# Kernel optimization log

Measured on AMD Instinct MI355X. Metric: run time of the kernel, lower is better.

The kernel has to match this reference:

```python
import jax, jax.numpy as jnp
import numpy as np
import math

B, S, D, H = 2, 2048, 1024, 16
DK = D // H

def setup_inputs() -> dict:
    key = jax.random.key(0)
    ks = jax.random.split(key, 12)
    std = 1.0 / math.sqrt(D)
    inp = {
        'query': jax.random.normal(ks[0], (B, S, D), jnp.float32),
        'key':   jax.random.normal(ks[1], (B, S, D), jnp.float32),
        'value': jax.random.normal(ks[2], (B, S, D), jnp.float32),
        'mask':  jnp.ones((B, 1, 1, S), dtype=bool),
        'wq': jax.random.normal(ks[3], (D, D), jnp.float32) * std,
        'bq': jnp.zeros((D,), jnp.float32),
        'wk': jax.random.normal(ks[4], (D, D), jnp.float32) * std,
        'bk': jnp.zeros((D,), jnp.float32),
        'wv': jax.random.normal(ks[5], (D, D), jnp.float32) * std,
        'bv': jnp.zeros((D,), jnp.float32),
        'wo': jax.random.normal(ks[6], (D, D), jnp.float32) * std,
        'bo': jnp.zeros((D,), jnp.float32),
    }
    return inp

def reference(query, key, value, mask, wq, bq, wk, bk, wv, bv, wo, bo):
    # torch.nn.Linear: y = x @ W^T + b
    def split_heads(x):  # [B,S,D] -> [B,H,S,DK]
        return x.reshape(B, -1, H, DK).transpose(0, 2, 1, 3)
    Q = split_heads(query @ wq.T + bq)
    K = split_heads(key @ wk.T + bk)
    V = split_heads(value @ wv.T + bv)
    scale = 1.0 / math.sqrt(DK)
    scores = jnp.einsum('bhtd,bhsd->bhts', Q, K * scale)  # [B,H,S,S]
    scores = jnp.where(mask, scores, -jnp.inf)
    attn = jax.nn.softmax(scores, axis=-1)
    # dropout p=0.0 (eval) -> identity
    context = jnp.einsum('bhts,bhsd->bhtd', attn, V)
    context = context.transpose(0, 2, 1, 3).reshape(B, -1, D)
    return context @ wo.T + bo
```

## Files before the change

kernel.cpp:

```cpp
#include <hip/hip_runtime.h>
#include <stdint.h>

#define SEQ 2048
#define NH  16

typedef __bf16 bf16x8 __attribute__((ext_vector_type(8)));
typedef float  f32x4  __attribute__((ext_vector_type(4)));
typedef float  f32x16 __attribute__((ext_vector_type(16)));
typedef unsigned uint2v __attribute__((ext_vector_type(2)));

#if __has_builtin(__builtin_amdgcn_exp2f)
#define EXP2(x) __builtin_amdgcn_exp2f(x)
#else
#define EXP2(x) exp2f(x)
#endif

#define WAITV0 asm volatile("s_waitcnt vmcnt(0)" ::: "memory")
#define WAITV4 asm volatile("s_waitcnt vmcnt(4)" ::: "memory")
#define SBAR() do { __builtin_amdgcn_sched_barrier(0); __builtin_amdgcn_s_barrier(); __builtin_amdgcn_sched_barrier(0); } while (0)

__device__ __forceinline__ unsigned short f2bf(float f) {
  union { float f; uint32_t u; } v; v.f = f;
  uint32_t r = v.u + 0x7fffu + ((v.u >> 16) & 1u);
  return (unsigned short)(r >> 16);
}

__device__ __forceinline__ void gll16(const void* g, void* l) {
  __builtin_amdgcn_global_load_lds((const __attribute__((address_space(1))) void*)g,
                                   (__attribute__((address_space(3))) void*)l, 16, 0, 0);
}

__device__ __forceinline__ f32x4 mfma16(bf16x8 a, bf16x8 b, f32x4 c) {
  return __builtin_amdgcn_mfma_f32_16x16x32_bf16(a, b, c, 0, 0, 0);
}
__device__ __forceinline__ f32x16 mfma32(bf16x8 a, bf16x8 b, f32x16 c) {
  return __builtin_amdgcn_mfma_f32_32x32x16_bf16(a, b, c, 0, 0, 0);
}

struct CvtJobs {
  const float* s[7];
  unsigned short* d[7];
  int n4[7];
};

__global__ void cvt_all(CvtJobs J) {
  int j = blockIdx.y;
  const float* __restrict__ s = J.s[j];
  unsigned short* __restrict__ d = J.d[j];
  int n4 = J.n4[j];
  int st = gridDim.x * blockDim.x;
  for (int i = blockIdx.x * blockDim.x + threadIdx.x; i < n4; i += st) {
    float4 v = ((const float4*)s)[i];
    union { unsigned short u[4]; uint2 q; } o;
    o.u[0] = f2bf(v.x); o.u[1] = f2bf(v.y); o.u[2] = f2bf(v.z); o.u[3] = f2bf(v.w);
    ((uint2*)d)[i] = o.q;
  }
}

struct GemmJobs {
  const unsigned short* A[3];
  const unsigned short* W[3];
  const float* bias[3];
  void* out[3];
  float scale[3];
  int mode[3];
};

template<int BM, int NB>
__global__ __launch_bounds__(256, (BM == 128 ? 3 : 2)) void gemm_t(GemmJobs J) {
  __shared__ alignas(16) unsigned short Asm[BM * 64];
  __shared__ alignas(16) unsigned short Bsm[128 * 64];
  constexpr int MFR = BM / 32;
  constexpr int MB = 4096 / BM;
  const int tid = threadIdx.x;
  const int l = tid & 63, w = tid >> 6;
  const int wr = w >> 1, wc = w & 1;
  const int lg = l >> 4, lo = l & 15;

  const int nwg = gridDim.x;
  const int id = blockIdx.x;
  const int swz = (id & 7) * (nwg >> 3) + (id >> 3);
  const int g = swz / NB;
  const int rem = swz % NB;
  const int m0 = (rem % MB) * BM;
  const int n0 = (rem / MB) * 128;

  const unsigned short* __restrict__ A = J.A[g];
  const unsigned short* __restrict__ W = J.W[g];
  const float* __restrict__ bias = J.bias[g];
  const int mode = J.mode[g];
  const float scale = J.scale[g];

  f32x4 acc[MFR][4] = {};

  for (int kt = 0; kt < 16; ++kt) {
#pragma unroll
    for (int it = 0; it < BM / 32; ++it) {
      int chunk = it * 256 + tid;
      int row = chunk >> 3, c = chunk & 7;
      const char* src = (const char*)A + (((size_t)(m0 + row) << 10) + (kt << 6)) * 2 + ((c ^ (row & 7)) << 4);
      gll16(src, (char*)Asm + ((it * 256 + (tid & ~63)) << 4));
    }
#pragma unroll
    for (int it = 0; it < 4; ++it) {
      int chunk = it * 256 + tid;
      int row = chunk >> 3, c = chunk & 7;
      const char* src = (const char*)W + (((size_t)(n0 + row) << 10) + (kt << 6)) * 2 + ((c ^ (row & 7)) << 4);
      gll16(src, (char*)Bsm + ((it * 256 + (tid & ~63)) << 4));
    }
    WAITV0;
    SBAR();
#pragma unroll
    for (int kf = 0; kf < 2; ++kf) {
      bf16x8 af[MFR], bfr[4];
#pragma unroll
      for (int mf = 0; mf < MFR; ++mf) {
        int row = wr * (BM / 2) + mf * 16 + lo;
        int pos = (kf * 4 + lg) ^ (row & 7);
        af[mf] = *(const bf16x8*)((const char*)Asm + row * 128 + pos * 16);
      }
#pragma unroll
      for (int nf = 0; nf < 4; ++nf) {
        int row = wc * 64 + nf * 16 + lo;
        int pos = (kf * 4 + lg) ^ (row & 7);
        bfr[nf] = *(const bf16x8*)((const char*)Bsm + row * 128 + pos * 16);
      }
#pragma unroll
      for (int mf = 0; mf < MFR; ++mf)
#pragma unroll
        for (int nf = 0; nf < 4; ++nf)
          acc[mf][nf] = mfma16(af[mf], bfr[nf], acc[mf][nf]);
    }
    SBAR();
  }

#pragma unroll
  for (int mf = 0; mf < MFR; ++mf)
#pragma unroll
    for (int nf = 0; nf < 4; ++nf) {
      int gcol = n0 + wc * 64 + nf * 16 + lo;
      float bv = bias[gcol];
#pragma unroll
      for (int r = 0; r < 4; ++r) {
        int grow = m0 + wr * (BM / 2) + mf * 16 + lg * 4 + r;
        float v = (acc[mf][nf][r] + bv) * scale;
        if (mode == 2) {
          ((float*)J.out[g])[((size_t)grow << 10) + gcol] = v;
        } else {
          int b = grow >> 11, s = grow & 2047, h = gcol >> 6, dk = gcol & 63;
          size_t idx;
          if (mode == 0) idx = ((((size_t)((b << 4) + h) << 11) + s) << 6) + dk;
          else           idx = ((((size_t)((b << 4) + h) << 6) + dk) << 11) + s;
          ((__bf16*)J.out[g])[idx] = (__bf16)v;
        }
      }
    }
}

__global__ __launch_bounds__(256, 2) void attn_kernel(const unsigned short* __restrict__ Qb,
                                                      const unsigned short* __restrict__ Kb,
                                                      const unsigned short* __restrict__ Vt,
                                                      unsigned short* __restrict__ ctx) {
  __shared__ alignas(16) unsigned short Ksm[2][64 * 64];
  __shared__ alignas(16) unsigned short Vsm[2][64 * 64];
  const int tid = threadIdx.x;
  const int l = tid & 63, w = tid >> 6;
  const int ql = l & 31, hi = l >> 5;

  const int id = blockIdx.x;
  const int swz = (id & 7) * 64 + (id >> 3);
  const int bh = swz >> 4;
  const int qt = swz & 15;

  const unsigned short* Qp = Qb + (size_t)bh * SEQ * 64;
  const unsigned short* Kp = Kb + (size_t)bh * SEQ * 64;
  const unsigned short* Vp = Vt + (size_t)bh * 64 * SEQ;
  const int q0 = qt * 128 + w * 32;

  bf16x8 qb[4];
#pragma unroll
  for (int c = 0; c < 4; ++c)
    qb[c] = *(const bf16x8*)((const char*)Qp + (((size_t)(q0 + ql)) << 7) + c * 32 + hi * 16);
  WAITV0;

  f32x16 o0 = {}, o1 = {};
  float m_ = -1e30f, l_ = 0.f;

#define ASTAGE(b, t)                                                                      \
  do {                                                                                    \
    const int kv0s = (t) << 6;                                                            \
    _Pragma("unroll")                                                                     \
    for (int it = 0; it < 2; ++it) {                                                      \
      int chunk = it * 256 + tid;                                                         \
      int row = chunk >> 3, c = chunk & 7;                                                \
      const char* ksrc = (const char*)Kp + ((size_t)(kv0s + row) << 7) + ((c ^ (row & 7)) << 4); \
      gll16(ksrc, (char*)Ksm[b] + ((it * 256 + (tid & ~63)) << 4));                       \
      const char* vsrc = (const char*)Vp + ((size_t)row << 12) + (kv0s << 1) + ((c ^ (row & 7)) << 4); \
      gll16(vsrc, (char*)Vsm[b] + ((it * 256 + (tid & ~63)) << 4));                       \
    }                                                                                     \
  } while (0)

  ASTAGE(0, 0);

  for (int t = 0; t < SEQ / 64; ++t) {
    const int cur = t & 1;
    if (t < SEQ / 64 - 1) {
      ASTAGE(cur ^ 1, t + 1);
      WAITV4;
    } else {
      WAITV0;
    }
    SBAR();

    f32x16 s0 = {}, s1 = {};
    __builtin_amdgcn_s_setprio(1);
#pragma unroll
    for (int c = 0; c < 4; ++c) {
      int pr = c * 2 + hi;
      bf16x8 k0 = *(const bf16x8*)((const char*)Ksm[cur] + ql * 128 + ((pr ^ (ql & 7)) << 4));
      bf16x8 k1 = *(const bf16x8*)((const char*)Ksm[cur] + (32 + ql) * 128 + ((pr ^ ((32 + ql) & 7)) << 4));
      s0 = mfma32(k0, qb[c], s0);
      s1 = mfma32(k1, qb[c], s1);
    }
    __builtin_amdgcn_s_setprio(0);

#define MAX4(v, i) fmaxf(fmaxf(v[i], v[i+1]), fmaxf(v[i+2], v[i+3]))
    float mA = fmaxf(fmaxf(MAX4(s0, 0), MAX4(s0, 4)), fmaxf(MAX4(s0, 8), MAX4(s0, 12)));
    float mB = fmaxf(fmaxf(MAX4(s1, 0), MAX4(s1, 4)), fmaxf(MAX4(s1, 8), MAX4(s1, 12)));
    float mx = fmaxf(mA, mB);
    mx = fmaxf(mx, __shfl_xor(mx, 32));
#undef MAX4

    if (__any((int)(mx > m_))) {
      float mnew = fmaxf(m_, mx);
      float fac = EXP2(m_ - mnew);
      m_ = mnew;
#pragma unroll
      for (int r = 0; r < 16; ++r) { s0[r] = EXP2(s0[r] - mnew); s1[r] = EXP2(s1[r] - mnew); }
#define SUM4(v, i) ((v[i] + v[i+1]) + (v[i+2] + v[i+3]))
      float ps = ((SUM4(s0, 0) + SUM4(s0, 4)) + (SUM4(s0, 8) + SUM4(s0, 12)))
               + ((SUM4(s1, 0) + SUM4(s1, 4)) + (SUM4(s1, 8) + SUM4(s1, 12)));
      ps += __shfl_xor(ps, 32);
      l_ = l_ * fac + ps;
#pragma unroll
      for (int reg = 0; reg < 16; ++reg) {
        int qrow = (reg & 3) + 8 * (reg >> 2) + 4 * hi;
        float fb = __shfl(fac, qrow);
        o0[reg] *= fb; o1[reg] *= fb;
      }
    } else {
#pragma unroll
      for (int r = 0; r < 16; ++r) { s0[r] = EXP2(s0[r] - m_); s1[r] = EXP2(s1[r] - m_); }
      float ps = ((SUM4(s0, 0) + SUM4(s0, 4)) + (SUM4(s0, 8) + SUM4(s0, 12)))
               + ((SUM4(s1, 0) + SUM4(s1, 4)) + (SUM4(s1, 8) + SUM4(s1, 12)));
      ps += __shfl_xor(ps, 32);
      l_ += ps;
#undef SUM4
    }

    bf16x8 pa[4];
#pragma unroll
    for (int c = 0; c < 4; ++c) {
      const int rb = (c & 1) * 8;
      float e0, e1, e2, e3, e4, e5, e6, e7;
      if ((c >> 1) == 0) { e0=s0[rb]; e1=s0[rb+1]; e2=s0[rb+2]; e3=s0[rb+3]; e4=s0[rb+4]; e5=s0[rb+5]; e6=s0[rb+6]; e7=s0[rb+7]; }
      else               { e0=s1[rb]; e1=s1[rb+1]; e2=s1[rb+2]; e3=s1[rb+3]; e4=s1[rb+4]; e5=s1[rb+5]; e6=s1[rb+6]; e7=s1[rb+7]; }
      unsigned X0, X1, Z0, Z1;
      asm("v_cvt_pk_bf16_f32 %0, %1, %2" : "=v"(X0) : "v"(e0), "v"(e1));
      asm("v_cvt_pk_bf16_f32 %0, %1, %2" : "=v"(X1) : "v"(e2), "v"(e3));
      asm("v_cvt_pk_bf16_f32 %0, %1, %2" : "=v"(Z0) : "v"(e4), "v"(e5));
      asm("v_cvt_pk_bf16_f32 %0, %1, %2" : "=v"(Z1) : "v"(e6), "v"(e7));
      uint2v rA = __builtin_amdgcn_permlane32_swap(X0, Z0, false, false);
      uint2v rB = __builtin_amdgcn_permlane32_swap(X1, Z1, false, false);
      union { unsigned u[4]; bf16x8 v; } pk_;
      pk_.u[0] = rA[0]; pk_.u[1] = rB[0]; pk_.u[2] = rA[1]; pk_.u[3] = rB[1];
      pa[c] = pk_.v;
    }

    __builtin_amdgcn_s_setprio(1);
#pragma unroll
    for (int c = 0; c < 4; ++c) {
      int pr = c * 2 + hi;
      bf16x8 v0 = *(const bf16x8*)((const char*)Vsm[cur] + ql * 128 + ((pr ^ (ql & 7)) << 4));
      bf16x8 v1 = *(const bf16x8*)((const char*)Vsm[cur] + (32 + ql) * 128 + ((pr ^ ((32 + ql) & 7)) << 4));
      o0 = mfma32(pa[c], v0, o0);
      o1 = mfma32(pa[c], v1, o1);
    }
    __builtin_amdgcn_s_setprio(0);
    SBAR();
  }
#undef ASTAGE

  const int b = bh >> 4, h = bh & 15;
#pragma unroll
  for (int reg = 0; reg < 16; ++reg) {
    int qrow = (reg & 3) + 8 * (reg >> 2) + 4 * hi;
    float lr = __shfl(l_, qrow);
    float inv = 1.f / lr;
    int srow = q0 + qrow;
    size_t off = (((size_t)(b * SEQ + srow)) << 10) + h * 64 + ql;
    ((__bf16*)ctx)[off]      = (__bf16)(o0[reg] * inv);
    ((__bf16*)ctx)[off + 32] = (__bf16)(o1[reg] * inv);
  }
}

extern "C" void kernel_launch(void* const* d_in, const int* in_sizes, int n_in,
                              void* d_out, int out_size, void* d_ws, size_t ws_size,
                              hipStream_t stream) {
  const float* query = (const float*)d_in[0];
  const float* key_  = (const float*)d_in[1];
  const float* value = (const float*)d_in[2];
  const float* wq = (const float*)d_in[4];
  const float* bq = (const float*)d_in[5];
  const float* wk = (const float*)d_in[6];
  const float* bk = (const float*)d_in[7];
  const float* wv = (const float*)d_in[8];
  const float* bv = (const float*)d_in[9];
  const float* wo = (const float*)d_in[10];
  const float* bo = (const float*)d_in[11];

  char* ws = (char*)d_ws;
  unsigned short* xq  = (unsigned short*)(ws + 0);
  unsigned short* xk  = (unsigned short*)(ws + 8388608);
  unsigned short* xv  = (unsigned short*)(ws + 16777216);
  unsigned short* wqb = (unsigned short*)(ws + 25165824);
  unsigned short* wkb = (unsigned short*)(ws + 27262976);
  unsigned short* wvb = (unsigned short*)(ws + 29360128);
  unsigned short* wob = (unsigned short*)(ws + 31457280);
  unsigned short* Qb  = (unsigned short*)(ws + 33554432);
  unsigned short* Kb  = (unsigned short*)(ws + 41943040);
  unsigned short* Vb  = (unsigned short*)(ws + 50331648);
  unsigned short* ctx = (unsigned short*)(ws + 58720256);

  CvtJobs cj;
  cj.s[0] = query; cj.d[0] = xq;  cj.n4[0] = 1048576;
  cj.s[1] = key_;  cj.d[1] = xk;  cj.n4[1] = 1048576;
  cj.s[2] = value; cj.d[2] = xv;  cj.n4[2] = 1048576;
  cj.s[3] = wq;    cj.d[3] = wqb; cj.n4[3] = 262144;
  cj.s[4] = wk;    cj.d[4] = wkb; cj.n4[4] = 262144;
  cj.s[5] = wv;    cj.d[5] = wvb; cj.n4[5] = 262144;
  cj.s[6] = wo;    cj.d[6] = wob; cj.n4[6] = 262144;
  cvt_all<<<dim3(256, 7), 256, 0, stream>>>(cj);

  const float kscale = 0.125f * 1.44269504088896340736f;
  GemmJobs gj;
  gj.A[0] = xq; gj.W[0] = wqb; gj.bias[0] = bq; gj.out[0] = (void*)Qb; gj.scale[0] = 1.0f;   gj.mode[0] = 0;
  gj.A[1] = xk; gj.W[1] = wkb; gj.bias[1] = bk; gj.out[1] = (void*)Kb; gj.scale[1] = kscale; gj.mode[1] = 0;
  gj.A[2] = xv; gj.W[2] = wvb; gj.bias[2] = bv; gj.out[2] = (void*)Vb; gj.scale[2] = 1.0f;   gj.mode[2] = 1;
  gemm_t<128, 256><<<768, 256, 0, stream>>>(gj);

  attn_kernel<<<512, 256, 0, stream>>>(Qb, Kb, Vb, ctx);

  GemmJobs oj;
  oj.A[0] = ctx; oj.W[0] = wob; oj.bias[0] = bo; oj.out[0] = d_out; oj.scale[0] = 1.0f; oj.mode[0] = 2;
  oj.A[1] = oj.A[0]; oj.W[1] = oj.W[0]; oj.bias[1] = oj.bias[0]; oj.out[1] = oj.out[0]; oj.scale[1] = 1.0f; oj.mode[1] = 2;
  oj.A[2] = oj.A[0]; oj.W[2] = oj.W[0]; oj.bias[2] = oj.bias[0]; oj.out[2] = oj.out[0]; oj.scale[2] = 1.0f; oj.mode[2] = 2;
  gemm_t<64, 512><<<512, 256, 0, stream>>>(oj);
}
```

Baseline: 150.4 us.

## Software-pipeline QK^T one tile ahead of softmax and PV in attention loop

Restructures the flash-attention main loop so the QK^T MFMAs for the next KV tile are issued before the softmax and PV of the current tile, with the loop unrolled by two over the double buffers. The aim is to overlap MFMA work with the exp/max/convert VALU work. It also adds a lazy rescale threshold (the max is updated only when it grows by more than 8 in log2 units) and fmax3-based reductions. The costs are higher register pressure from holding two score tiles, and a stricter wait (vmcnt(0)) placed right before each barrier, which may expose load latency.

```diff
diff --git a/kernel.cpp b/kernel.cpp
--- a/kernel.cpp
+++ b/kernel.cpp
@@ -16,13 +16,16 @@
 #endif
 
 #define WAITV0 asm volatile("s_waitcnt vmcnt(0)" ::: "memory")
-#define WAITV4 asm volatile("s_waitcnt vmcnt(4)" ::: "memory")
 #define SBAR() do { __builtin_amdgcn_sched_barrier(0); __builtin_amdgcn_s_barrier(); __builtin_amdgcn_sched_barrier(0); } while (0)
 
 __device__ __forceinline__ unsigned short f2bf(float f) {
   union { float f; uint32_t u; } v; v.f = f;
   uint32_t r = v.u + 0x7fffu + ((v.u >> 16) & 1u);
   return (unsigned short)(r >> 16);
+}
+
+__device__ __forceinline__ float fmax3(float a, float b, float c) {
+  return fmaxf(fmaxf(a, b), c);
 }
 
 __device__ __forceinline__ void gll16(const void* g, void* l) {
@@ -200,48 +203,32 @@
     }                                                                                     \
   } while (0)
 
-  ASTAGE(0, 0);
-
-  for (int t = 0; t < SEQ / 64; ++t) {
-    const int cur = t & 1;
-    if (t < SEQ / 64 - 1) {
-      ASTAGE(cur ^ 1, t + 1);
-      WAITV4;
-    } else {
-      WAITV0;
-    }
-    SBAR();
-
-    f32x16 s0 = {}, s1 = {};
+  auto QKT = [&](int buf, f32x16& t0, f32x16& t1) {
+    t0 = (f32x16){}; t1 = (f32x16){};
     __builtin_amdgcn_s_setprio(1);
 #pragma unroll
     for (int c = 0; c < 4; ++c) {
       int pr = c * 2 + hi;
-      bf16x8 k0 = *(const bf16x8*)((const char*)Ksm[cur] + ql * 128 + ((pr ^ (ql & 7)) << 4));
-      bf16x8 k1 = *(const bf16x8*)((const char*)Ksm[cur] + (32 + ql) * 128 + ((pr ^ ((32 + ql) & 7)) << 4));
-      s0 = mfma32(k0, qb[c], s0);
-      s1 = mfma32(k1, qb[c], s1);
+      bf16x8 k0 = *(const bf16x8*)((const char*)Ksm[buf] + ql * 128 + ((pr ^ (ql & 7)) << 4));
+      bf16x8 k1 = *(const bf16x8*)((const char*)Ksm[buf] + (32 + ql) * 128 + ((pr ^ ((32 + ql) & 7)) << 4));
+      t0 = mfma32(k0, qb[c], t0);
+      t1 = mfma32(k1, qb[c], t1);
     }
     __builtin_amdgcn_s_setprio(0);
-
-#define MAX4(v, i) fmaxf(fmaxf(v[i], v[i+1]), fmaxf(v[i+2], v[i+3]))
-    float mA = fmaxf(fmaxf(MAX4(s0, 0), MAX4(s0, 4)), fmaxf(MAX4(s0, 8), MAX4(s0, 12)));
-    float mB = fmaxf(fmaxf(MAX4(s1, 0), MAX4(s1, 4)), fmaxf(MAX4(s1, 8), MAX4(s1, 12)));
-    float mx = fmaxf(mA, mB);
+  };
+
+  auto SMPA = [&](f32x16& s0, f32x16& s1, bf16x8* pa) {
+#define MAX8(v, i) fmax3(fmax3(v[i], v[i+1], v[i+2]), fmax3(v[i+3], v[i+4], v[i+5]), fmaxf(v[i+6], v[i+7]))
+    float mx = fmaxf(fmaxf(MAX8(s0, 0), MAX8(s0, 8)), fmaxf(MAX8(s1, 0), MAX8(s1, 8)));
     mx = fmaxf(mx, __shfl_xor(mx, 32));
-#undef MAX4
-
-    if (__any((int)(mx > m_))) {
+#undef MAX8
+    if (__builtin_expect(__any((int)(mx > m_ + 8.f)), 0)) {
       float mnew = fmaxf(m_, mx);
       float fac = EXP2(m_ - mnew);
       m_ = mnew;
 #pragma unroll
       for (int r = 0; r < 16; ++r) { s0[r] = EXP2(s0[r] - mnew); s1[r] = EXP2(s1[r] - mnew); }
-#define SUM4(v, i) ((v[i] + v[i+1]) + (v[i+2] + v[i+3]))
-      float ps = ((SUM4(s0, 0) + SUM4(s0, 4)) + (SUM4(s0, 8) + SUM4(s0, 12)))
-               + ((SUM4(s1, 0) + SUM4(s1, 4)) + (SUM4(s1, 8) + SUM4(s1, 12)));
-      ps += __shfl_xor(ps, 32);
-      l_ = l_ * fac + ps;
+      l_ *= fac;
 #pragma unroll
       for (int reg = 0; reg < 16; ++reg) {
         int qrow = (reg & 3) + 8 * (reg >> 2) + 4 * hi;
@@ -251,14 +238,13 @@
     } else {
 #pragma unroll
       for (int r = 0; r < 16; ++r) { s0[r] = EXP2(s0[r] - m_); s1[r] = EXP2(s1[r] - m_); }
-      float ps = ((SUM4(s0, 0) + SUM4(s0, 4)) + (SUM4(s0, 8) + SUM4(s0, 12)))
-               + ((SUM4(s1, 0) + SUM4(s1, 4)) + (SUM4(s1, 8) + SUM4(s1, 12)));
-      ps += __shfl_xor(ps, 32);
-      l_ += ps;
+    }
+#define SUM4(v, i) ((v[i] + v[i+1]) + (v[i+2] + v[i+3]))
+    float ps = ((SUM4(s0, 0) + SUM4(s0, 4)) + (SUM4(s0, 8) + SUM4(s0, 12)))
+             + ((SUM4(s1, 0) + SUM4(s1, 4)) + (SUM4(s1, 8) + SUM4(s1, 12)));
 #undef SUM4
-    }
-
-    bf16x8 pa[4];
+    ps += __shfl_xor(ps, 32);
+    l_ += ps;
 #pragma unroll
     for (int c = 0; c < 4; ++c) {
       const int rb = (c & 1) * 8;
@@ -276,19 +262,51 @@
       pk_.u[0] = rA[0]; pk_.u[1] = rB[0]; pk_.u[2] = rA[1]; pk_.u[3] = rB[1];
       pa[c] = pk_.v;
     }
-
+  };
+
+  auto PV = [&](int buf, bf16x8* pa) {
     __builtin_amdgcn_s_setprio(1);
 #pragma unroll
     for (int c = 0; c < 4; ++c) {
       int pr = c * 2 + hi;
-      bf16x8 v0 = *(const bf16x8*)((const char*)Vsm[cur] + ql * 128 + ((pr ^ (ql & 7)) << 4));
-      bf16x8 v1 = *(const bf16x8*)((const char*)Vsm[cur] + (32 + ql) * 128 + ((pr ^ ((32 + ql) & 7)) << 4));
+      bf16x8 v0 = *(const bf16x8*)((const char*)Vsm[buf] + ql * 128 + ((pr ^ (ql & 7)) << 4));
+      bf16x8 v1 = *(const bf16x8*)((const char*)Vsm[buf] + (32 + ql) * 128 + ((pr ^ ((32 + ql) & 7)) << 4));
       o0 = mfma32(pa[c], v0, o0);
       o1 = mfma32(pa[c], v1, o1);
     }
     __builtin_amdgcn_s_setprio(0);
+  };
+
+  f32x16 sA0, sA1, sB0, sB1;
+  bf16x8 pa[4];
+
+  ASTAGE(0, 0);
+  WAITV0; SBAR();
+  QKT(0, sA0, sA1);
+  ASTAGE(1, 1);
+
+  for (int tp = 0; tp < 15; ++tp) {
+    const int te = tp * 2;
+    WAITV0; SBAR();
+    QKT(1, sB0, sB1);
+    SMPA(sA0, sA1, pa);
+    PV(0, pa);
     SBAR();
+    ASTAGE(0, te + 2);
+    WAITV0; SBAR();
+    QKT(0, sA0, sA1);
+    SMPA(sB0, sB1, pa);
+    PV(1, pa);
+    SBAR();
+    ASTAGE(1, te + 3);
   }
+  WAITV0; SBAR();
+  QKT(1, sB0, sB1);
+  SMPA(sA0, sA1, pa);
+  PV(0, pa);
+  SMPA(sB0, sB1, pa);
+  PV(1, pa);
+
 #undef ASTAGE
 
   const int b = bh >> 4, h = bh & 15;
```

New measurement: 326.5 us. 2.17x slower.

## Split attention KV range across two blocks and merge with a combine kernel

Applied to the files above, without the earlier changes.

Attention is split-KV: each of 1024 blocks handles half of the key sequence and writes unnormalized fp32 partial outputs plus per-row max and sum into scratch (d_out and reused workspace). A new combine kernel rescales and merges the two halves into bf16 context. This doubles the grid and raises the occupancy bound to fill more CUs. The online softmax also rescales only when the max grows by more than 8 (in log2 units), and the row sum is hoisted out of both branches. The costs are the extra partial-buffer traffic and one more launch.

```diff
diff --git a/kernel.cpp b/kernel.cpp
--- a/kernel.cpp
+++ b/kernel.cpp
@@ -23,6 +23,10 @@
   union { float f; uint32_t u; } v; v.f = f;
   uint32_t r = v.u + 0x7fffu + ((v.u >> 16) & 1u);
   return (unsigned short)(r >> 16);
+}
+
+__device__ __forceinline__ float fmax3(float a, float b, float c) {
+  return fmaxf(fmaxf(a, b), c);
 }
 
 __device__ __forceinline__ void gll16(const void* g, void* l) {
@@ -157,10 +161,12 @@
     }
 }
 
-__global__ __launch_bounds__(256, 2) void attn_kernel(const unsigned short* __restrict__ Qb,
-                                                      const unsigned short* __restrict__ Kb,
-                                                      const unsigned short* __restrict__ Vt,
-                                                      unsigned short* __restrict__ ctx) {
+__global__ __launch_bounds__(256, 4) void attn_split(const unsigned short* __restrict__ Qb,
+                                                     const unsigned short* __restrict__ Kb,
+                                                     const unsigned short* __restrict__ Vt,
+                                                     float* __restrict__ part0,
+                                                     float* __restrict__ part1,
+                                                     float* __restrict__ ml) {
   __shared__ alignas(16) unsigned short Ksm[2][64 * 64];
   __shared__ alignas(16) unsigned short Vsm[2][64 * 64];
   const int tid = threadIdx.x;
@@ -168,9 +174,11 @@
   const int ql = l & 31, hi = l >> 5;
 
   const int id = blockIdx.x;
-  const int swz = (id & 7) * 64 + (id >> 3);
-  const int bh = swz >> 4;
+  const int swz = (id & 7) * 128 + (id >> 3);
+  const int half = swz >> 9;
+  const int bh = (swz >> 4) & 31;
   const int qt = swz & 15;
+  const int t0 = half * 16;
 
   const unsigned short* Qp = Qb + (size_t)bh * SEQ * 64;
   const unsigned short* Kp = Kb + (size_t)bh * SEQ * 64;
@@ -200,12 +208,12 @@
     }                                                                                     \
   } while (0)
 
-  ASTAGE(0, 0);
-
-  for (int t = 0; t < SEQ / 64; ++t) {
+  ASTAGE(0, t0);
+
+  for (int t = 0; t < 16; ++t) {
     const int cur = t & 1;
-    if (t < SEQ / 64 - 1) {
-      ASTAGE(cur ^ 1, t + 1);
+    if (t < 15) {
+      ASTAGE(cur ^ 1, t0 + t + 1);
       WAITV4;
     } else {
       WAITV0;
@@ -224,24 +232,17 @@
     }
     __builtin_amdgcn_s_setprio(0);
 
-#define MAX4(v, i) fmaxf(fmaxf(v[i], v[i+1]), fmaxf(v[i+2], v[i+3]))
-    float mA = fmaxf(fmaxf(MAX4(s0, 0), MAX4(s0, 4)), fmaxf(MAX4(s0, 8), MAX4(s0, 12)));
-    float mB = fmaxf(fmaxf(MAX4(s1, 0), MAX4(s1, 4)), fmaxf(MAX4(s1, 8), MAX4(s1, 12)));
-    float mx = fmaxf(mA, mB);
+#define MAX8(v, i) fmax3(fmax3(v[i], v[i+1], v[i+2]), fmax3(v[i+3], v[i+4], v[i+5]), fmaxf(v[i+6], v[i+7]))
+    float mx = fmaxf(fmaxf(MAX8(s0, 0), MAX8(s0, 8)), fmaxf(MAX8(s1, 0), MAX8(s1, 8)));
     mx = fmaxf(mx, __shfl_xor(mx, 32));
-#undef MAX4
-
-    if (__any((int)(mx > m_))) {
+#undef MAX8
+    if (__builtin_expect(__any((int)(mx > m_ + 8.f)), 0)) {
       float mnew = fmaxf(m_, mx);
       float fac = EXP2(m_ - mnew);
       m_ = mnew;
 #pragma unroll
       for (int r = 0; r < 16; ++r) { s0[r] = EXP2(s0[r] - mnew); s1[r] = EXP2(s1[r] - mnew); }
-#define SUM4(v, i) ((v[i] + v[i+1]) + (v[i+2] + v[i+3]))
-      float ps = ((SUM4(s0, 0) + SUM4(s0, 4)) + (SUM4(s0, 8) + SUM4(s0, 12)))
-               + ((SUM4(s1, 0) + SUM4(s1, 4)) + (SUM4(s1, 8) + SUM4(s1, 12)));
-      ps += __shfl_xor(ps, 32);
-      l_ = l_ * fac + ps;
+      l_ *= fac;
 #pragma unroll
       for (int reg = 0; reg < 16; ++reg) {
         int qrow = (reg & 3) + 8 * (reg >> 2) + 4 * hi;
@@ -251,12 +252,13 @@
     } else {
 #pragma unroll
       for (int r = 0; r < 16; ++r) { s0[r] = EXP2(s0[r] - m_); s1[r] = EXP2(s1[r] - m_); }
-      float ps = ((SUM4(s0, 0) + SUM4(s0, 4)) + (SUM4(s0, 8) + SUM4(s0, 12)))
-               + ((SUM4(s1, 0) + SUM4(s1, 4)) + (SUM4(s1, 8) + SUM4(s1, 12)));
-      ps += __shfl_xor(ps, 32);
-      l_ += ps;
+    }
+#define SUM4(v, i) ((v[i] + v[i+1]) + (v[i+2] + v[i+3]))
+    float ps = ((SUM4(s0, 0) + SUM4(s0, 4)) + (SUM4(s0, 8) + SUM4(s0, 12)))
+             + ((SUM4(s1, 0) + SUM4(s1, 4)) + (SUM4(s1, 8) + SUM4(s1, 12)));
 #undef SUM4
-    }
+    ps += __shfl_xor(ps, 32);
+    l_ += ps;
 
     bf16x8 pa[4];
 #pragma unroll
@@ -291,16 +293,46 @@
   }
 #undef ASTAGE
 
-  const int b = bh >> 4, h = bh & 15;
+  const int bhqt = bh * 16 + qt;
+  const int idx = bhqt * 2 + half;
+  float* pb = (half ? part1 : part0) + (size_t)bhqt * 8192;
 #pragma unroll
   for (int reg = 0; reg < 16; ++reg) {
     int qrow = (reg & 3) + 8 * (reg >> 2) + 4 * hi;
-    float lr = __shfl(l_, qrow);
-    float inv = 1.f / lr;
-    int srow = q0 + qrow;
-    size_t off = (((size_t)(b * SEQ + srow)) << 10) + h * 64 + ql;
-    ((__bf16*)ctx)[off]      = (__bf16)(o0[reg] * inv);
-    ((__bf16*)ctx)[off + 32] = (__bf16)(o1[reg] * inv);
+    int qloc = w * 32 + qrow;
+    pb[qloc * 64 + ql]      = o0[reg];
+    pb[qloc * 64 + 32 + ql] = o1[reg];
+  }
+  if (hi == 0) {
+    ml[idx * 256 + w * 32 + ql]       = m_;
+    ml[idx * 256 + 128 + w * 32 + ql] = l_;
+  }
+}
+
+__global__ __launch_bounds__(256, 8) void attn_combine(const float* __restrict__ part0,
+                                                       const float* __restrict__ part1,
+                                                       const float* __restrict__ ml,
+                                                       unsigned short* __restrict__ ctx) {
+  const int bhqt = blockIdx.x;
+  const int bh = bhqt >> 4, qt = bhqt & 15;
+  const int b = bh >> 4, h = bh & 15;
+  const int dk = threadIdx.x & 63;
+  const int q4 = threadIdx.x >> 6;
+  const int i0 = bhqt * 2, i1 = bhqt * 2 + 1;
+  const float* p0 = part0 + (size_t)bhqt * 8192;
+  const float* p1 = part1 + (size_t)bhqt * 8192;
+#pragma unroll 4
+  for (int qq = 0; qq < 32; ++qq) {
+    int q = qq * 4 + q4;
+    float m1 = ml[i0 * 256 + q], l1 = ml[i0 * 256 + 128 + q];
+    float m2 = ml[i1 * 256 + q], l2 = ml[i1 * 256 + 128 + q];
+    float M = fmaxf(m1, m2);
+    float f1 = EXP2(m1 - M), f2 = EXP2(m2 - M);
+    float L = l1 * f1 + l2 * f2;
+    float inv = 1.f / L;
+    float v = (p0[q * 64 + dk] * f1 + p1[q * 64 + dk] * f2) * inv;
+    int s = qt * 128 + q;
+    ((__bf16*)ctx)[(((size_t)(b * SEQ + s)) << 10) + h * 64 + dk] = (__bf16)v;
   }
 }
 
@@ -332,6 +364,10 @@
   unsigned short* Vb  = (unsigned short*)(ws + 50331648);
   unsigned short* ctx = (unsigned short*)(ws + 58720256);
 
+  float* part0 = (float*)d_out;
+  float* part1 = (float*)(ws + 0);
+  float* mlbuf = (float*)(ws + 16777216);
+
   CvtJobs cj;
   cj.s[0] = query; cj.d[0] = xq;  cj.n4[0] = 1048576;
   cj.s[1] = key_;  cj.d[1] = xk;  cj.n4[1] = 1048576;
@@ -349,7 +385,8 @@
   gj.A[2] = xv; gj.W[2] = wvb; gj.bias[2] = bv; gj.out[2] = (void*)Vb; gj.scale[2] = 1.0f;   gj.mode[2] = 1;
   gemm_t<128, 256><<<768, 256, 0, stream>>>(gj);
 
-  attn_kernel<<<512, 256, 0, stream>>>(Qb, Kb, Vb, ctx);
+  attn_split<<<1024, 256, 0, stream>>>(Qb, Kb, Vb, part0, part1, mlbuf);
+  attn_combine<<<512, 256, 0, stream>>>(part0, part1, mlbuf, ctx);
 
   GemmJobs oj;
   oj.A[0] = ctx; oj.W[0] = wob; oj.bias[0] = bo; oj.out[0] = d_out; oj.scale[0] = 1.0f; oj.mode[0] = 2;
```

Result: slower. 228.6 us (+52.0%).
